# Kernel optimization log

Measured on AMD Instinct MI355X. Metric: run time of the kernel, lower is better.

The kernel has to match this reference:

```python
import jax, jax.numpy as jnp
import numpy as np

N = 50000      # nodes
E = 1_600_000  # edges (before self-loops)
G = 100        # graphs in batch
IN = 16        # in_channels
H1, C1 = 4, 32 # gat1 heads, per-head channels
H2, C2 = 1, 32 # gat2 heads, per-head channels
NEG_SLOPE = 0.2


def setup_inputs() -> dict:
    key = jax.random.key(0)
    ks = jax.random.split(key, 16)
    s = 0.1
    return {
        "x": jax.random.normal(ks[0], (N, IN), jnp.float32),
        "edge_index": jax.random.randint(ks[1], (2, E), 0, N, dtype=jnp.int64),
        "batch": jnp.sort(jax.random.randint(ks[2], (N,), 0, G, dtype=jnp.int64)),
        # GATConv 1: lin (no bias), att_src/att_dst, output bias (concat -> H1*C1)
        "W1": jax.random.normal(ks[3], (IN, H1 * C1), jnp.float32) * s,
        "att_src1": jax.random.normal(ks[4], (H1, C1), jnp.float32) * s,
        "att_dst1": jax.random.normal(ks[5], (H1, C1), jnp.float32) * s,
        "b1": jnp.zeros((H1 * C1,), jnp.float32),
        # GATConv 2
        "W2": jax.random.normal(ks[6], (H1 * C1, H2 * C2), jnp.float32) * s,
        "att_src2": jax.random.normal(ks[7], (H2, C2), jnp.float32) * s,
        "att_dst2": jax.random.normal(ks[8], (H2, C2), jnp.float32) * s,
        "b2": jnp.zeros((H2 * C2,), jnp.float32),
        # MLP head: Linear(32,64) -> ReLU -> Linear(64,1)
        "Wh1": jax.random.normal(ks[9], (C2, 64), jnp.float32) * s,
        "bh1": jnp.zeros((64,), jnp.float32),
        "Wh2": jax.random.normal(ks[10], (64, 1), jnp.float32) * s,
        "bh2": jnp.zeros((1,), jnp.float32),
    }


def gat_conv(x, src, dst, W, a_src, a_dst, bias, heads, ch):
    """PyG GATConv (self-loops already included in src/dst), eval mode."""
    n = x.shape[0]
    h = (x @ W).reshape(n, heads, ch)                 # [N,H,C]
    # per-node attention logits, then gather per edge
    a_s = jnp.einsum('nhc,hc->nh', h, a_src)          # [N,H]
    a_d = jnp.einsum('nhc,hc->nh', h, a_dst)
    e = jax.nn.leaky_relu(a_s[src] + a_d[dst], NEG_SLOPE)  # [E,H]
    # segment softmax over incoming edges of each destination node
    m = jax.ops.segment_max(e, dst, num_segments=n)   # [N,H]
    ex = jnp.exp(e - m[dst])
    denom = jax.ops.segment_sum(ex, dst, num_segments=n)
    alpha = ex / (denom[dst] + 1e-16)                 # [E,H]
    # weighted scatter-aggregate of source features
    out = jax.ops.segment_sum(alpha[:, :, None] * h[src], dst, num_segments=n)
    return out.reshape(n, heads * ch) + bias


def reference(x, edge_index, batch, W1, att_src1, att_dst1, b1,
              W2, att_src2, att_dst2, b2, Wh1, bh1, Wh2, bh2):
    n = x.shape[0]
    loops = jnp.arange(n, dtype=edge_index.dtype)
    src = jnp.concatenate([edge_index[0], loops])
    dst = jnp.concatenate([edge_index[1], loops])

    h = jax.nn.elu(gat_conv(x, src, dst, W1, att_src1, att_dst1, b1, H1, C1))
    h = jax.nn.elu(gat_conv(h, src, dst, W2, att_src2, att_dst2, b2, H2, C2))

    # global mean pool by graph id
    sums = jax.ops.segment_sum(h, batch, num_segments=G)          # [G,C2]
    cnts = jax.ops.segment_sum(jnp.ones((n,), h.dtype), batch, num_segments=G)
    pooled = sums / jnp.maximum(cnts, 1.0)[:, None]

    out = jax.nn.relu(pooled @ Wh1 + bh1) @ Wh2 + bh2             # [G,1]
    return out
```

## Files before the change

kernel.cpp:

```cpp
#include <hip/hip_runtime.h>
#include <hip/hip_fp16.h>
#include <math.h>

#define IN_CH 16
#define HC1 128
#define NH1 4
#define C2 32
#define HID 64
#define NEG 0.2f
#define CAP 10240
#define CHUNK 4096

__device__ __forceinline__ float lrelu_exp(float z) {
    float lr = z > 0.f ? z : NEG * z;
    return expf(lr);
}

__global__ void k_bucket(const int* __restrict__ ei, int E, int N, int nbk,
                         int* __restrict__ cursors, int* __restrict__ buckets) {
    __shared__ int cnt[256];
    __shared__ int base[256];
    __shared__ int pos[256];
    int t = threadIdx.x;
    int c0 = blockIdx.x * CHUNK;
    int M = E + N;
    cnt[t] = 0;
    pos[t] = 0;
    __syncthreads();
    int srcv[16], dstv[16];
#pragma unroll
    for (int k = 0; k < 16; ++k) {
        int i = c0 + k * 256 + t;
        int s = -1, d = -1;
        if (i < M) {
            if (i < E) { s = ei[i]; d = ei[E + i]; }
            else       { s = d = i - E; }
            atomicAdd(&cnt[d >> 8], 1);
        }
        srcv[k] = s; dstv[k] = d;
    }
    __syncthreads();
    if (cnt[t] > 0) base[t] = atomicAdd(&cursors[t], cnt[t]);
    __syncthreads();
#pragma unroll
    for (int k = 0; k < 16; ++k) {
        int d = dstv[k];
        if (d >= 0) {
            int b = d >> 8;
            int p = base[b] + atomicAdd(&pos[b], 1);
            buckets[b * CAP + p] = (srcv[k] << 8) | (d & 255);
        }
    }
}

__global__ void k_bscan(const int* __restrict__ cursors, int nbk,
                        int* __restrict__ bbase, int* __restrict__ offsets,
                        int N, int M) {
    __shared__ int s[256];
    int t = threadIdx.x;
    int v = (t < nbk) ? cursors[t] : 0;
    s[t] = v;
    __syncthreads();
    for (int o = 1; o < 256; o <<= 1) {
        int a = (t >= o) ? s[t - o] : 0;
        __syncthreads();
        s[t] += a;
        __syncthreads();
    }
    bbase[t] = s[t] - v;
    if (t == 0) offsets[N] = M;
}

__global__ void k_build(const int* __restrict__ buckets, const int* __restrict__ cursors,
                        const int* __restrict__ bbase, int N,
                        int* __restrict__ offsets, int* __restrict__ elist) {
    __shared__ int deg[256];
    __shared__ int sc[256];
    __shared__ int cur[256];
    int b = blockIdx.x, t = threadIdx.x;
    int n0 = b << 8;
    int cnt = cursors[b];
    int gbase = bbase[b];
    const int* bk = buckets + b * CAP;
    deg[t] = 0;
    __syncthreads();
    for (int i = t; i < cnt; i += 256) atomicAdd(&deg[bk[i] & 255], 1);
    __syncthreads();
    int v = deg[t];
    sc[t] = v;
    __syncthreads();
    for (int o = 1; o < 256; o <<= 1) {
        int a = (t >= o) ? sc[t - o] : 0;
        __syncthreads();
        sc[t] += a;
        __syncthreads();
    }
    int excl = sc[t] - v;
    cur[t] = excl;
    if (n0 + t < N) offsets[n0 + t] = gbase + excl;
    __syncthreads();
    for (int i = t; i < cnt; i += 256) {
        int e = bk[i];
        int p = atomicAdd(&cur[e & 255], 1);
        elist[gbase + p] = e >> 8;
    }
}

__global__ void k_lin1(const float* __restrict__ x, const float2* __restrict__ W1v,
                       const float2* __restrict__ att_s2, const float2* __restrict__ att_d2,
                       int N, __half2* __restrict__ h1h, float* __restrict__ as1, float* __restrict__ ad1) {
    int wave = threadIdx.x >> 6;
    int lane = threadIdx.x & 63;
    int n = blockIdx.x * 4 + wave;
    if (n >= N) return;
    float xv = x[n * IN_CH + (lane & 15)];
    float ax = 0.f, ay = 0.f;
#pragma unroll
    for (int k = 0; k < IN_CH; ++k) {
        float xk = __shfl(xv, k, 16);
        float2 w = W1v[k * 64 + lane];
        ax += xk * w.x;
        ay += xk * w.y;
    }
    h1h[(size_t)n * 64 + lane] = __floats2half2_rn(ax, ay);
    float2 s2 = att_s2[lane], d2 = att_d2[lane];
    float vs = ax * s2.x + ay * s2.y;
    float vd = ax * d2.x + ay * d2.y;
#pragma unroll
    for (int o = 1; o < 16; o <<= 1) {
        vs += __shfl_xor(vs, o, 64);
        vd += __shfl_xor(vd, o, 64);
    }
    if ((lane & 15) == 0) {
        as1[n * NH1 + (lane >> 4)] = vs;
        ad1[n * NH1 + (lane >> 4)] = vd;
    }
}

__global__ void k_agg1(const int* __restrict__ offsets, const int* __restrict__ elist,
                       const float* __restrict__ as1, const float* __restrict__ ad1,
                       const float4* __restrict__ h1q, const float* __restrict__ b1,
                       int N, float4* __restrict__ out1q) {
    int wave = threadIdx.x >> 6;
    int lane = threadIdx.x & 63;
    int n = blockIdx.x * 4 + wave;
    if (n >= N) return;
    int slot = lane >> 4, chunk = lane & 15, head = chunk >> 2;
    int lo = offsets[n], hi = offsets[n + 1];
    float adh = ad1[n * NH1 + head];
    float acc[8];
#pragma unroll
    for (int j = 0; j < 8; ++j) acc[j] = 0.f;
    float sumw = 0.f;
#pragma unroll 2
    for (int e0 = lo; e0 < hi; e0 += 8) {
        int eA = e0 + slot, eB = e0 + 4 + slot;
        bool okA = eA < hi, okB = eB < hi;
        int sA = elist[okA ? eA : lo];
        int sB = elist[okB ? eB : lo];
        float zA = as1[sA * NH1 + head];
        float zB = as1[sB * NH1 + head];
        float4 vA = h1q[(size_t)sA * 16 + chunk];
        float4 vB = h1q[(size_t)sB * 16 + chunk];
        float wA = okA ? lrelu_exp(zA + adh) : 0.f;
        float wB = okB ? lrelu_exp(zB + adh) : 0.f;
        const __half2* hA = (const __half2*)&vA;
        const __half2* hB = (const __half2*)&vB;
#pragma unroll
        for (int j = 0; j < 4; ++j) {
            float2 fA = __half22float2(hA[j]);
            float2 fB = __half22float2(hB[j]);
            acc[2 * j]     += wA * fA.x + wB * fB.x;
            acc[2 * j + 1] += wA * fA.y + wB * fB.y;
        }
        sumw += wA + wB;
    }
#pragma unroll
    for (int j = 0; j < 8; ++j) {
        acc[j] += __shfl_xor(acc[j], 16, 64);
        acc[j] += __shfl_xor(acc[j], 32, 64);
    }
    sumw += __shfl_xor(sumw, 16, 64);
    sumw += __shfl_xor(sumw, 32, 64);
    if (slot == 0) {
        float inv = 1.f / (sumw + 1e-16f);
        float4 ba = ((const float4*)b1)[2 * chunk];
        float4 bb = ((const float4*)b1)[2 * chunk + 1];
        float o[8];
        o[0] = acc[0] * inv + ba.x; o[1] = acc[1] * inv + ba.y;
        o[2] = acc[2] * inv + ba.z; o[3] = acc[3] * inv + ba.w;
        o[4] = acc[4] * inv + bb.x; o[5] = acc[5] * inv + bb.y;
        o[6] = acc[6] * inv + bb.z; o[7] = acc[7] * inv + bb.w;
#pragma unroll
        for (int j = 0; j < 8; ++j) o[j] = o[j] > 0.f ? o[j] : expm1f(o[j]);
        float4 pk;
        __half2* ph = (__half2*)&pk;
        ph[0] = __floats2half2_rn(o[0], o[1]);
        ph[1] = __floats2half2_rn(o[2], o[3]);
        ph[2] = __floats2half2_rn(o[4], o[5]);
        ph[3] = __floats2half2_rn(o[6], o[7]);
        out1q[(size_t)n * 16 + chunk] = pk;
    }
}

#define TN 64
__global__ void k_lin2(const __half2* __restrict__ out1h, const float* __restrict__ W2,
                       const float* __restrict__ att_s, const float* __restrict__ att_d,
                       int N, __half2* __restrict__ h2h, float* __restrict__ as2, float* __restrict__ ad2) {
    __shared__ float sx[TN][HC1 + 1];
    __shared__ float sw[HC1][C2];
    int t = threadIdx.x;
    int base = blockIdx.x * TN;
    int lim = (N - base) * HC1;
    for (int i = t * 4; i < HC1 * C2; i += 1024) {
        float4 v = *(const float4*)(W2 + i);
        sw[i >> 5][i & 31] = v.x;
        sw[i >> 5][(i & 31) + 1] = v.y;
        sw[i >> 5][(i & 31) + 2] = v.z;
        sw[i >> 5][(i & 31) + 3] = v.w;
    }
    for (int i = t * 4; i < TN * HC1; i += 1024) {
        float2 a = make_float2(0.f, 0.f), b = make_float2(0.f, 0.f);
        if (i < lim) {
            size_t idx = ((size_t)base * HC1 + i) >> 1;
            a = __half22float2(out1h[idx]);
            b = __half22float2(out1h[idx + 1]);
        }
        int nn = i >> 7, kk = i & 127;
        sx[nn][kk] = a.x; sx[nn][kk + 1] = a.y; sx[nn][kk + 2] = b.x; sx[nn][kk + 3] = b.y;
    }
    __syncthreads();
    int nloc = t >> 2;
    int c0 = (t & 3) * 8;
    float acc[8];
#pragma unroll
    for (int j = 0; j < 8; ++j) acc[j] = 0.f;
#pragma unroll 4
    for (int k = 0; k < HC1; ++k) {
        float xv = sx[nloc][k];
        float4 wa = *(float4*)&sw[k][c0];
        float4 wb = *(float4*)&sw[k][c0 + 4];
        acc[0] += xv * wa.x; acc[1] += xv * wa.y; acc[2] += xv * wa.z; acc[3] += xv * wa.w;
        acc[4] += xv * wb.x; acc[5] += xv * wb.y; acc[6] += xv * wb.z; acc[7] += xv * wb.w;
    }
    int n = base + nloc;
    if (n < N) {
#pragma unroll
        for (int j = 0; j < 4; ++j)
            h2h[(size_t)n * 16 + (c0 >> 1) + j] = __floats2half2_rn(acc[2 * j], acc[2 * j + 1]);
        float ps = 0.f, pd = 0.f;
#pragma unroll
        for (int j = 0; j < 8; ++j) {
            ps += acc[j] * att_s[c0 + j];
            pd += acc[j] * att_d[c0 + j];
        }
        ps += __shfl_down(ps, 1, 64); ps += __shfl_down(ps, 2, 64);
        pd += __shfl_down(pd, 1, 64); pd += __shfl_down(pd, 2, 64);
        if ((t & 3) == 0) { as2[n] = ps; ad2[n] = pd; }
    }
}

__global__ void k_agg2(const int* __restrict__ offsets, const int* __restrict__ elist,
                       const float* __restrict__ as2, const float* __restrict__ ad2,
                       const float4* __restrict__ h2q, const float* __restrict__ b2,
                       int N, float* __restrict__ out2) {
    int wave = threadIdx.x >> 6;
    int lane = threadIdx.x & 63;
    int n = blockIdx.x * 4 + wave;
    if (n >= N) return;
    int slot = lane >> 2, chunk = lane & 3;
    int lo = offsets[n], hi = offsets[n + 1];
    float ad = ad2[n];
    float acc[8];
#pragma unroll
    for (int j = 0; j < 8; ++j) acc[j] = 0.f;
    float sumw = 0.f;
    for (int e0 = lo; e0 < hi; e0 += 32) {
        int eA = e0 + slot, eB = e0 + 16 + slot;
        bool okA = eA < hi, okB = eB < hi;
        int sA = elist[okA ? eA : lo];
        int sB = elist[okB ? eB : lo];
        float zA = as2[sA];
        float zB = as2[sB];
        float4 vA = h2q[(size_t)sA * 4 + chunk];
        float4 vB = h2q[(size_t)sB * 4 + chunk];
        float wA = okA ? lrelu_exp(zA + ad) : 0.f;
        float wB = okB ? lrelu_exp(zB + ad) : 0.f;
        const __half2* hA = (const __half2*)&vA;
        const __half2* hB = (const __half2*)&vB;
#pragma unroll
        for (int j = 0; j < 4; ++j) {
            float2 fA = __half22float2(hA[j]);
            float2 fB = __half22float2(hB[j]);
            acc[2 * j]     += wA * fA.x + wB * fB.x;
            acc[2 * j + 1] += wA * fA.y + wB * fB.y;
        }
        sumw += wA + wB;
    }
#pragma unroll
    for (int j = 0; j < 8; ++j) {
        acc[j] += __shfl_xor(acc[j], 4, 64);
        acc[j] += __shfl_xor(acc[j], 8, 64);
        acc[j] += __shfl_xor(acc[j], 16, 64);
        acc[j] += __shfl_xor(acc[j], 32, 64);
    }
    sumw += __shfl_xor(sumw, 4, 64);
    sumw += __shfl_xor(sumw, 8, 64);
    sumw += __shfl_xor(sumw, 16, 64);
    sumw += __shfl_xor(sumw, 32, 64);
    if (slot == 0) {
        float inv = 1.f / (sumw + 1e-16f);
        float4 ba = ((const float4*)b2)[2 * chunk];
        float4 bb = ((const float4*)b2)[2 * chunk + 1];
        float o[8];
        o[0] = acc[0] * inv + ba.x; o[1] = acc[1] * inv + ba.y;
        o[2] = acc[2] * inv + ba.z; o[3] = acc[3] * inv + ba.w;
        o[4] = acc[4] * inv + bb.x; o[5] = acc[5] * inv + bb.y;
        o[6] = acc[6] * inv + bb.z; o[7] = acc[7] * inv + bb.w;
#pragma unroll
        for (int j = 0; j < 8; ++j) o[j] = o[j] > 0.f ? o[j] : expm1f(o[j]);
        float* dst = out2 + (size_t)n * C2 + 8 * chunk;
        *(float4*)dst = make_float4(o[0], o[1], o[2], o[3]);
        *(float4*)(dst + 4) = make_float4(o[4], o[5], o[6], o[7]);
    }
}

__global__ void k_pool(const float* __restrict__ out2, const int* __restrict__ batch,
                       int N, const float* __restrict__ Wh1, const float* __restrict__ bh1,
                       const float* __restrict__ Wh2, const float* __restrict__ bh2,
                       float* __restrict__ out) {
    int g = blockIdx.x;
    int t = threadIdx.x;
    __shared__ int sb[2];
    __shared__ float pooled[C2];
    __shared__ float red[256];
    if (t < 2) {
        int target = g + t;
        int lo = 0, hi = N;
        while (lo < hi) { int mid = (lo + hi) >> 1; if (batch[mid] < target) lo = mid + 1; else hi = mid; }
        sb[t] = lo;
    }
    __syncthreads();
    int lo = sb[0], hi = sb[1];
    int c = t & 31, grp = t >> 5;
    float part = 0.f;
    for (int n = lo + grp; n < hi; n += 8) part += out2[n * C2 + c];
    red[t] = part;
    __syncthreads();
    if (t < 128) red[t] += red[t + 128];
    __syncthreads();
    if (t < 64) red[t] += red[t + 64];
    __syncthreads();
    if (t < 32) {
        red[t] += red[t + 32];
        float cnt = (float)(hi - lo);
        pooled[t] = red[t] / fmaxf(cnt, 1.f);
    }
    __syncthreads();
    float hval = 0.f;
    if (t < HID) {
        float a = bh1[t];
#pragma unroll
        for (int cc = 0; cc < C2; ++cc) a += pooled[cc] * Wh1[cc * HID + t];
        hval = fmaxf(a, 0.f) * Wh2[t];
    }
    if (t < 64) {
        for (int o = 32; o > 0; o >>= 1) hval += __shfl_down(hval, o, 64);
        if (t == 0) out[g] = hval + bh2[0];
    }
}

extern "C" void kernel_launch(void* const* d_in, const int* in_sizes, int n_in,
                              void* d_out, int out_size, void* d_ws, size_t ws_size,
                              hipStream_t stream) {
    const float* x    = (const float*)d_in[0];
    const int*   ei   = (const int*)d_in[1];
    const int*   batch= (const int*)d_in[2];
    const float* W1   = (const float*)d_in[3];
    const float* aS1  = (const float*)d_in[4];
    const float* aD1  = (const float*)d_in[5];
    const float* b1   = (const float*)d_in[6];
    const float* W2   = (const float*)d_in[7];
    const float* aS2  = (const float*)d_in[8];
    const float* aD2  = (const float*)d_in[9];
    const float* b2   = (const float*)d_in[10];
    const float* Wh1  = (const float*)d_in[11];
    const float* bh1  = (const float*)d_in[12];
    const float* Wh2  = (const float*)d_in[13];
    const float* bh2  = (const float*)d_in[14];
    float* out = (float*)d_out;

    int N = in_sizes[2];
    int E = in_sizes[1] / 2;
    int M = E + N;
    int G = out_size;
    int nbk = (N + 255) >> 8;

    char* p = (char*)d_ws;
    auto alloc = [&](size_t bytes) -> void* {
        void* r = (void*)p;
        p += (bytes + 255) & ~(size_t)255;
        return r;
    };
    __half2* h1h   = (__half2*)alloc((size_t)N * 64 * 4);
    __half2* out1h = (__half2*)alloc((size_t)N * 64 * 4);
    __half2* h2h   = (__half2*)alloc((size_t)N * 16 * 4);
    float* as1     = (float*)alloc((size_t)N * NH1 * 4);
    float* ad1     = (float*)alloc((size_t)N * NH1 * 4);
    float* as2     = (float*)alloc((size_t)N * 4);
    float* ad2     = (float*)alloc((size_t)N * 4);
    float* out2    = (float*)alloc((size_t)N * C2 * 4);
    int*   offsets = (int*)alloc((size_t)(N + 1) * 4);
    int*   elist   = (int*)alloc((size_t)M * 4);
    int*   cursors = (int*)alloc(256 * 4);
    int*   bbase   = (int*)alloc(256 * 4);
    int*   buckets = (int*)alloc((size_t)nbk * CAP * 4);

    hipMemsetAsync(cursors, 0, 256 * 4, stream);
    k_bucket<<<(M + CHUNK - 1) / CHUNK, 256, 0, stream>>>(ei, E, N, nbk, cursors, buckets);
    k_bscan<<<1, 256, 0, stream>>>(cursors, nbk, bbase, offsets, N, M);
    k_build<<<nbk, 256, 0, stream>>>(buckets, cursors, bbase, N, offsets, elist);
    k_lin1<<<(N + 3) / 4, 256, 0, stream>>>(x, (const float2*)W1, (const float2*)aS1,
                                            (const float2*)aD1, N, h1h, as1, ad1);
    k_agg1<<<(N + 3) / 4, 256, 0, stream>>>(offsets, elist, as1, ad1,
                                            (const float4*)h1h, b1, N, (float4*)out1h);
    k_lin2<<<(N + TN - 1) / TN, 256, 0, stream>>>(out1h, W2, aS2, aD2, N, h2h, as2, ad2);
    k_agg2<<<(N + 3) / 4, 256, 0, stream>>>(offsets, elist, as2, ad2,
                                            (const float4*)h2h, b2, N, out2);
    k_pool<<<G, 256, 0, stream>>>(out2, batch, N, Wh1, bh1, Wh2, bh2, out);
}
```

Before: 294.4 us.

## Fuse bucketing with lin1, fold scan into build, unroll edge gathers

The edge bucketing kernel and the first linear layer are merged into one launch that splits its blocks by index, so the two independent jobs run together. The bucket-offset scan moves into k_build, where every block redoes the 256-entry scan, which removes the separate single-block k_bscan launch. Both aggregation kernels issue four (agg1) or two (agg2) independent neighbour gathers per iteration, computing addresses from byte offsets so more loads are in flight at once. They also use the fast __expf intrinsic, trading a little accuracy for fewer instructions and adding some register pressure.

```diff
diff --git a/kernel.cpp b/kernel.cpp
--- a/kernel.cpp
+++ b/kernel.cpp
@@ -11,78 +11,103 @@
 #define CAP 10240
 #define CHUNK 4096
 
-__device__ __forceinline__ float lrelu_exp(float z) {
-    float lr = z > 0.f ? z : NEG * z;
-    return expf(lr);
-}
-
-__global__ void k_bucket(const int* __restrict__ ei, int E, int N, int nbk,
-                         int* __restrict__ cursors, int* __restrict__ buckets) {
-    __shared__ int cnt[256];
-    __shared__ int base[256];
-    __shared__ int pos[256];
-    int t = threadIdx.x;
-    int c0 = blockIdx.x * CHUNK;
-    int M = E + N;
-    cnt[t] = 0;
-    pos[t] = 0;
-    __syncthreads();
-    int srcv[16], dstv[16];
-#pragma unroll
-    for (int k = 0; k < 16; ++k) {
-        int i = c0 + k * 256 + t;
-        int s = -1, d = -1;
-        if (i < M) {
-            if (i < E) { s = ei[i]; d = ei[E + i]; }
-            else       { s = d = i - E; }
-            atomicAdd(&cnt[d >> 8], 1);
-        }
-        srcv[k] = s; dstv[k] = d;
-    }
-    __syncthreads();
-    if (cnt[t] > 0) base[t] = atomicAdd(&cursors[t], cnt[t]);
-    __syncthreads();
-#pragma unroll
-    for (int k = 0; k < 16; ++k) {
-        int d = dstv[k];
-        if (d >= 0) {
-            int b = d >> 8;
-            int p = base[b] + atomicAdd(&pos[b], 1);
-            buckets[b * CAP + p] = (srcv[k] << 8) | (d & 255);
-        }
-    }
-}
-
-__global__ void k_bscan(const int* __restrict__ cursors, int nbk,
-                        int* __restrict__ bbase, int* __restrict__ offsets,
-                        int N, int M) {
-    __shared__ int s[256];
-    int t = threadIdx.x;
-    int v = (t < nbk) ? cursors[t] : 0;
-    s[t] = v;
-    __syncthreads();
-    for (int o = 1; o < 256; o <<= 1) {
-        int a = (t >= o) ? s[t - o] : 0;
-        __syncthreads();
-        s[t] += a;
-        __syncthreads();
-    }
-    bbase[t] = s[t] - v;
-    if (t == 0) offsets[N] = M;
+__device__ __forceinline__ float lrelu_exp_fast(float z) {
+    float lr = fmaxf(z, NEG * z);
+    return __expf(lr);
+}
+
+__global__ void k_front(const int* __restrict__ ei, int E, int N, int nchunk,
+                        int* __restrict__ cursors, int* __restrict__ buckets,
+                        const float* __restrict__ x, const float2* __restrict__ W1v,
+                        const float2* __restrict__ att_s2, const float2* __restrict__ att_d2,
+                        __half2* __restrict__ h1h, float* __restrict__ as1, float* __restrict__ ad1) {
+    int bid = blockIdx.x;
+    if (bid < nchunk) {
+        __shared__ int cnt[256];
+        __shared__ int base[256];
+        __shared__ int pos[256];
+        int t = threadIdx.x;
+        int c0 = bid * CHUNK;
+        int M = E + N;
+        cnt[t] = 0;
+        pos[t] = 0;
+        __syncthreads();
+        int srcv[16], dstv[16];
+#pragma unroll
+        for (int k = 0; k < 16; ++k) {
+            int i = c0 + k * 256 + t;
+            int s = -1, d = -1;
+            if (i < M) {
+                if (i < E) { s = ei[i]; d = ei[E + i]; }
+                else       { s = d = i - E; }
+                atomicAdd(&cnt[d >> 8], 1);
+            }
+            srcv[k] = s; dstv[k] = d;
+        }
+        __syncthreads();
+        if (cnt[t] > 0) base[t] = atomicAdd(&cursors[t], cnt[t]);
+        __syncthreads();
+#pragma unroll
+        for (int k = 0; k < 16; ++k) {
+            int d = dstv[k];
+            if (d >= 0) {
+                int b = d >> 8;
+                int p = base[b] + atomicAdd(&pos[b], 1);
+                buckets[b * CAP + p] = (srcv[k] << 8) | (d & 255);
+            }
+        }
+    } else {
+        int wave = threadIdx.x >> 6;
+        int lane = threadIdx.x & 63;
+        int n = (bid - nchunk) * 4 + wave;
+        if (n >= N) return;
+        float xv = x[n * IN_CH + (lane & 15)];
+        float ax = 0.f, ay = 0.f;
+#pragma unroll
+        for (int k = 0; k < IN_CH; ++k) {
+            float xk = __shfl(xv, k, 16);
+            float2 w = W1v[k * 64 + lane];
+            ax += xk * w.x;
+            ay += xk * w.y;
+        }
+        h1h[(size_t)n * 64 + lane] = __floats2half2_rn(ax, ay);
+        float2 s2 = att_s2[lane], d2 = att_d2[lane];
+        float vs = ax * s2.x + ay * s2.y;
+        float vd = ax * d2.x + ay * d2.y;
+#pragma unroll
+        for (int o = 1; o < 16; o <<= 1) {
+            vs += __shfl_xor(vs, o, 64);
+            vd += __shfl_xor(vd, o, 64);
+        }
+        if ((lane & 15) == 0) {
+            as1[n * NH1 + (lane >> 4)] = vs;
+            ad1[n * NH1 + (lane >> 4)] = vd;
+        }
+    }
 }
 
 __global__ void k_build(const int* __restrict__ buckets, const int* __restrict__ cursors,
-                        const int* __restrict__ bbase, int N,
+                        int N, int M,
                         int* __restrict__ offsets, int* __restrict__ elist) {
+    __shared__ int sc[256];
     __shared__ int deg[256];
-    __shared__ int sc[256];
     __shared__ int cur[256];
     int b = blockIdx.x, t = threadIdx.x;
+    int cv = cursors[t];
+    sc[t] = cv;
+    __syncthreads();
+    for (int o = 1; o < 256; o <<= 1) {
+        int a = (t >= o) ? sc[t - o] : 0;
+        __syncthreads();
+        sc[t] += a;
+        __syncthreads();
+    }
+    int cnt = cursors[b];
+    int gbase = sc[b] - cnt;
     int n0 = b << 8;
-    int cnt = cursors[b];
-    int gbase = bbase[b];
     const int* bk = buckets + b * CAP;
     deg[t] = 0;
+    if (b == 0 && t == 0) offsets[N] = M;
     __syncthreads();
     for (int i = t; i < cnt; i += 256) atomicAdd(&deg[bk[i] & 255], 1);
     __syncthreads();
@@ -106,40 +131,9 @@
     }
 }
 
-__global__ void k_lin1(const float* __restrict__ x, const float2* __restrict__ W1v,
-                       const float2* __restrict__ att_s2, const float2* __restrict__ att_d2,
-                       int N, __half2* __restrict__ h1h, float* __restrict__ as1, float* __restrict__ ad1) {
-    int wave = threadIdx.x >> 6;
-    int lane = threadIdx.x & 63;
-    int n = blockIdx.x * 4 + wave;
-    if (n >= N) return;
-    float xv = x[n * IN_CH + (lane & 15)];
-    float ax = 0.f, ay = 0.f;
-#pragma unroll
-    for (int k = 0; k < IN_CH; ++k) {
-        float xk = __shfl(xv, k, 16);
-        float2 w = W1v[k * 64 + lane];
-        ax += xk * w.x;
-        ay += xk * w.y;
-    }
-    h1h[(size_t)n * 64 + lane] = __floats2half2_rn(ax, ay);
-    float2 s2 = att_s2[lane], d2 = att_d2[lane];
-    float vs = ax * s2.x + ay * s2.y;
-    float vd = ax * d2.x + ay * d2.y;
-#pragma unroll
-    for (int o = 1; o < 16; o <<= 1) {
-        vs += __shfl_xor(vs, o, 64);
-        vd += __shfl_xor(vd, o, 64);
-    }
-    if ((lane & 15) == 0) {
-        as1[n * NH1 + (lane >> 4)] = vs;
-        ad1[n * NH1 + (lane >> 4)] = vd;
-    }
-}
-
 __global__ void k_agg1(const int* __restrict__ offsets, const int* __restrict__ elist,
-                       const float* __restrict__ as1, const float* __restrict__ ad1,
-                       const float4* __restrict__ h1q, const float* __restrict__ b1,
+                       const char* __restrict__ as1b, const float* __restrict__ ad1,
+                       const char* __restrict__ h1b, const float* __restrict__ b1,
                        int N, float4* __restrict__ out1q) {
     int wave = threadIdx.x >> 6;
     int lane = threadIdx.x & 63;
@@ -148,32 +142,39 @@
     int slot = lane >> 4, chunk = lane & 15, head = chunk >> 2;
     int lo = offsets[n], hi = offsets[n + 1];
     float adh = ad1[n * NH1 + head];
+    int coff = chunk << 4;
+    int hoff = head << 2;
     float acc[8];
 #pragma unroll
     for (int j = 0; j < 8; ++j) acc[j] = 0.f;
     float sumw = 0.f;
-#pragma unroll 2
-    for (int e0 = lo; e0 < hi; e0 += 8) {
-        int eA = e0 + slot, eB = e0 + 4 + slot;
-        bool okA = eA < hi, okB = eB < hi;
-        int sA = elist[okA ? eA : lo];
-        int sB = elist[okB ? eB : lo];
-        float zA = as1[sA * NH1 + head];
-        float zB = as1[sB * NH1 + head];
-        float4 vA = h1q[(size_t)sA * 16 + chunk];
-        float4 vB = h1q[(size_t)sB * 16 + chunk];
-        float wA = okA ? lrelu_exp(zA + adh) : 0.f;
-        float wB = okB ? lrelu_exp(zB + adh) : 0.f;
-        const __half2* hA = (const __half2*)&vA;
-        const __half2* hB = (const __half2*)&vB;
-#pragma unroll
-        for (int j = 0; j < 4; ++j) {
-            float2 fA = __half22float2(hA[j]);
-            float2 fB = __half22float2(hB[j]);
-            acc[2 * j]     += wA * fA.x + wB * fB.x;
-            acc[2 * j + 1] += wA * fA.y + wB * fB.y;
-        }
-        sumw += wA + wB;
+    for (int e0 = lo; e0 < hi; e0 += 16) {
+        int s[4]; bool ok[4]; float z[4]; float4 v[4]; float w[4];
+#pragma unroll
+        for (int u = 0; u < 4; ++u) {
+            int ee = e0 + 4 * u + slot;
+            ok[u] = ee < hi;
+            s[u] = elist[ok[u] ? ee : lo];
+        }
+#pragma unroll
+        for (int u = 0; u < 4; ++u) {
+            z[u] = *(const float*)(as1b + ((s[u] << 4) + hoff));
+            v[u] = *(const float4*)(h1b + ((s[u] << 8) + coff));
+        }
+#pragma unroll
+        for (int u = 0; u < 4; ++u)
+            w[u] = ok[u] ? lrelu_exp_fast(z[u] + adh) : 0.f;
+#pragma unroll
+        for (int u = 0; u < 4; ++u) {
+            const __half2* hv = (const __half2*)&v[u];
+#pragma unroll
+            for (int j = 0; j < 4; ++j) {
+                float2 f = __half22float2(hv[j]);
+                acc[2 * j]     += w[u] * f.x;
+                acc[2 * j + 1] += w[u] * f.y;
+            }
+            sumw += w[u];
+        }
     }
 #pragma unroll
     for (int j = 0; j < 8; ++j) {
@@ -261,8 +262,8 @@
 }
 
 __global__ void k_agg2(const int* __restrict__ offsets, const int* __restrict__ elist,
-                       const float* __restrict__ as2, const float* __restrict__ ad2,
-                       const float4* __restrict__ h2q, const float* __restrict__ b2,
+                       const char* __restrict__ as2b, const float* __restrict__ ad2,
+                       const char* __restrict__ h2b, const float* __restrict__ b2,
                        int N, float* __restrict__ out2) {
     int wave = threadIdx.x >> 6;
     int lane = threadIdx.x & 63;
@@ -271,31 +272,38 @@
     int slot = lane >> 2, chunk = lane & 3;
     int lo = offsets[n], hi = offsets[n + 1];
     float ad = ad2[n];
+    int coff = chunk << 4;
     float acc[8];
 #pragma unroll
     for (int j = 0; j < 8; ++j) acc[j] = 0.f;
     float sumw = 0.f;
     for (int e0 = lo; e0 < hi; e0 += 32) {
-        int eA = e0 + slot, eB = e0 + 16 + slot;
-        bool okA = eA < hi, okB = eB < hi;
-        int sA = elist[okA ? eA : lo];
-        int sB = elist[okB ? eB : lo];
-        float zA = as2[sA];
-        float zB = as2[sB];
-        float4 vA = h2q[(size_t)sA * 4 + chunk];
-        float4 vB = h2q[(size_t)sB * 4 + chunk];
-        float wA = okA ? lrelu_exp(zA + ad) : 0.f;
-        float wB = okB ? lrelu_exp(zB + ad) : 0.f;
-        const __half2* hA = (const __half2*)&vA;
-        const __half2* hB = (const __half2*)&vB;
-#pragma unroll
-        for (int j = 0; j < 4; ++j) {
-            float2 fA = __half22float2(hA[j]);
-            float2 fB = __half22float2(hB[j]);
-            acc[2 * j]     += wA * fA.x + wB * fB.x;
-            acc[2 * j + 1] += wA * fA.y + wB * fB.y;
-        }
-        sumw += wA + wB;
+        int s[2]; bool ok[2]; float z[2]; float4 v[2]; float w[2];
+#pragma unroll
+        for (int u = 0; u < 2; ++u) {
+            int ee = e0 + 16 * u + slot;
+            ok[u] = ee < hi;
+            s[u] = elist[ok[u] ? ee : lo];
+        }
+#pragma unroll
+        for (int u = 0; u < 2; ++u) {
+            z[u] = *(const float*)(as2b + (s[u] << 2));
+            v[u] = *(const float4*)(h2b + ((s[u] << 6) + coff));
+        }
+#pragma unroll
+        for (int u = 0; u < 2; ++u)
+            w[u] = ok[u] ? lrelu_exp_fast(z[u] + ad) : 0.f;
+#pragma unroll
+        for (int u = 0; u < 2; ++u) {
+            const __half2* hv = (const __half2*)&v[u];
+#pragma unroll
+            for (int j = 0; j < 4; ++j) {
+                float2 f = __half22float2(hv[j]);
+                acc[2 * j]     += w[u] * f.x;
+                acc[2 * j + 1] += w[u] * f.y;
+            }
+            sumw += w[u];
+        }
     }
 #pragma unroll
     for (int j = 0; j < 8; ++j) {
@@ -395,6 +403,8 @@
     int M = E + N;
     int G = out_size;
     int nbk = (N + 255) >> 8;
+    int nchunk = (M + CHUNK - 1) / CHUNK;
+    int nlin = (N + 3) / 4;
 
     char* p = (char*)d_ws;
     auto alloc = [&](size_t bytes) -> void* {
@@ -413,19 +423,17 @@
     int*   offsets = (int*)alloc((size_t)(N + 1) * 4);
     int*   elist   = (int*)alloc((size_t)M * 4);
     int*   cursors = (int*)alloc(256 * 4);
-    int*   bbase   = (int*)alloc(256 * 4);
     int*   buckets = (int*)alloc((size_t)nbk * CAP * 4);
 
     hipMemsetAsync(cursors, 0, 256 * 4, stream);
-    k_bucket<<<(M + CHUNK - 1) / CHUNK, 256, 0, stream>>>(ei, E, N, nbk, cursors, buckets);
-    k_bscan<<<1, 256, 0, stream>>>(cursors, nbk, bbase, offsets, N, M);
-    k_build<<<nbk, 256, 0, stream>>>(buckets, cursors, bbase, N, offsets, elist);
-    k_lin1<<<(N + 3) / 4, 256, 0, stream>>>(x, (const float2*)W1, (const float2*)aS1,
-                                            (const float2*)aD1, N, h1h, as1, ad1);
-    k_agg1<<<(N + 3) / 4, 256, 0, stream>>>(offsets, elist, as1, ad1,
-                                            (const float4*)h1h, b1, N, (float4*)out1h);
+    k_front<<<nchunk + nlin, 256, 0, stream>>>(ei, E, N, nchunk, cursors, buckets,
+                                               x, (const float2*)W1, (const float2*)aS1,
+                                               (const float2*)aD1, h1h, as1, ad1);
+    k_build<<<nbk, 256, 0, stream>>>(buckets, cursors, N, M, offsets, elist);
+    k_agg1<<<(N + 3) / 4, 256, 0, stream>>>(offsets, elist, (const char*)as1, ad1,
+                                            (const char*)h1h, b1, N, (float4*)out1h);
     k_lin2<<<(N + TN - 1) / TN, 256, 0, stream>>>(out1h, W2, aS2, aD2, N, h2h, as2, ad2);
-    k_agg2<<<(N + 3) / 4, 256, 0, stream>>>(offsets, elist, as2, ad2,
-                                            (const float4*)h2h, b2, N, out2);
+    k_agg2<<<(N + 3) / 4, 256, 0, stream>>>(offsets, elist, (const char*)as2, ad2,
+                                            (const char*)h2h, b2, N, out2);
     k_pool<<<G, 256, 0, stream>>>(out2, batch, N, Wh1, bh1, Wh2, bh2, out);
 }
```

Result: faster. 283.6 us (-3.7%).
